# Performance work log

Hardware: AMD Instinct MI355X
Metric: run time of the kernel (lower is better)

Reference implementation:

```python
import jax, jax.numpy as jnp
import numpy as np

B, D_IN, D_H, D_OUT, E = 8192, 512, 2048, 512, 8


def setup_inputs() -> dict:
    key = jax.random.key(0)
    k = jax.random.split(key, 6)
    return {
        "x": jax.random.normal(k[0], (B, D_IN), dtype=jnp.float32),
        "groups": jax.random.randint(k[1], (B, 1), 0, E, dtype=jnp.int64),
        "W1": jax.random.normal(k[2], (E, D_IN, D_H), dtype=jnp.float32) * (1.0 / np.sqrt(D_IN)),
        "b1": jnp.zeros((E, D_H), dtype=jnp.float32),
        "W2": jax.random.normal(k[3], (E, D_H, D_OUT), dtype=jnp.float32) * (1.0 / np.sqrt(D_H)),
        "b2": jnp.zeros((E, D_OUT), dtype=jnp.float32),
    }


def reference(x, groups, W1, b1, W2, b2):
    # SubnetGate: hard one-hot routing on group column 0, then weighted
    # combine (gate value is exactly 1.0 for the selected expert).
    n_expert = W1.shape[0]
    gate = jax.nn.one_hot(groups[:, 0], n_expert, dtype=x.dtype)  # [B, E]
    out = jnp.zeros((x.shape[0], W2.shape[-1]), dtype=x.dtype)
    # Loop over the small fixed expert set (structurally distinct subnets);
    # mask-combine reproduces dispatch -> subnet -> scatter/combine exactly.
    for e in range(n_expert):
        h = jax.nn.relu(x @ W1[e] + b1[e])        # [B, D_H]
        y = h @ W2[e] + b2[e]                      # [B, D_OUT]
        out = out + gate[:, e:e + 1] * y
    return out
```

## Files before the change

kernel.cpp:

```cpp
#include <hip/hip_runtime.h>
#include <hip/hip_bf16.h>

typedef unsigned short u16;
typedef __bf16 bf16x8 __attribute__((ext_vector_type(8)));
typedef float floatx4 __attribute__((ext_vector_type(4)));
typedef unsigned short ushort8 __attribute__((ext_vector_type(8)));

#define GLOBAL_AS(p) ((const __attribute__((address_space(1))) void*)(p))
#define LDS_AS(p) ((__attribute__((address_space(3))) void*)(p))

constexpr int NB = 8192;
constexpr int DIN = 512;
constexpr int DH = 2048;
constexpr int DOUT = 512;
constexpr int NEXP = 8;
constexpr int ROWCAP = NB + NEXP * 128;
constexpr int RCAPRD = NB + NEXP * 256;
constexpr int TILE = 8192;

__device__ __forceinline__ u16 f2bf(float f) {
    unsigned u = __builtin_bit_cast(unsigned, f);
    unsigned r = u + 0x7FFFu + ((u >> 16) & 1u);
    return (u16)(r >> 16);
}

__device__ __forceinline__ int slot_off(int row, int kl) {
    return row * 64 + ((((kl >> 3) ^ (row & 7)) << 3) | (kl & 7));
}

__global__ __launch_bounds__(1024) void route_kernel(
        const int* __restrict__ groups, int* __restrict__ cnt,
        int* __restrict__ offs, int* __restrict__ perm, int* __restrict__ rpos) {
    __shared__ int wc[NEXP * 16];
    __shared__ int lcur[NEXP * 16];
    int t = threadIdx.x;
    int w = t >> 6;
    if (t < NEXP * 16) wc[t] = 0;
    __syncthreads();
    for (int i = t; i < NB; i += 1024) atomicAdd(&wc[groups[i] * 16 + w], 1);
    __syncthreads();
    if (t == 0) {
        int run = 0;
        for (int e = 0; e < NEXP; ++e) {
            offs[e] = run;
            int s = run;
            for (int j = 0; j < 16; ++j) { lcur[e * 16 + j] = s; s += wc[e * 16 + j]; }
            cnt[e] = s - run;
            run += (((s - run) + 127) >> 7) << 7;
        }
    }
    __syncthreads();
    for (int i = t; i < NB; i += 1024) {
        int e = groups[i];
        int pos = atomicAdd(&lcur[e * 16 + w], 1);
        perm[pos] = i;
        rpos[i] = pos;
    }
}

__global__ __launch_bounds__(256) void prep_kernel(
        const float* __restrict__ x, const float* __restrict__ W1,
        const float* __restrict__ W2, const int* __restrict__ rpos,
        u16* __restrict__ xsT, u16* __restrict__ w1tT, u16* __restrict__ w2tT) {
    int bx = blockIdx.x;
    int t = threadIdx.x;
    if (bx < 4096) {
        __shared__ float tile[64][65];
        bool isW1 = bx < 2048;
        int b = isW1 ? bx : bx - 2048;
        int e = b >> 8;
        int q = b & 255;
        int C = isW1 ? DH : DOUT;
        int NTP = C >> 7;
        int KTP = isW1 ? (DIN >> 6) : (DH >> 6);
        int rt = isW1 ? (q >> 5) : (q >> 3);
        int ct = isW1 ? (q & 31) : (q & 7);
        const float* s = (isW1 ? W1 : W2) + (size_t)e * (isW1 ? DIN * DH : DH * DOUT);
        u16* d = isW1 ? w1tT : w2tT;
        int r0 = rt * 64, c0 = ct * 64;
        for (int i = 0; i < 4; ++i) {
            int r = (t >> 4) + i * 16;
            int c = (t & 15) * 4;
            const float4 v = *(const float4*)&s[(size_t)(r0 + r) * C + c0 + c];
            tile[r][c] = v.x; tile[r][c + 1] = v.y; tile[r][c + 2] = v.z; tile[r][c + 3] = v.w;
        }
        __syncthreads();
        for (int i = 0; i < 2; ++i) {
            int c = (t >> 3) + i * 32;
            int r = (t & 7) * 8;
            int n = c0 + c, k = r0 + r;
            ushort8 o;
#pragma unroll
            for (int j = 0; j < 8; ++j) o[j] = f2bf(tile[r + j][c]);
            size_t off = ((size_t)(e * NTP + (n >> 7)) * KTP + (k >> 6)) * TILE
                         + slot_off(n & 127, k & 63);
            *(ushort8*)&d[off] = o;
        }
    } else {
        int r = t >> 6, lane = t & 63;
        int i = (bx - 4096) * 4 + r;
        int pos = rpos[i];
        int k = lane * 8;
        const float4 a = *(const float4*)&x[(size_t)i * DIN + k];
        const float4 b = *(const float4*)&x[(size_t)i * DIN + k + 4];
        ushort8 o;
        o[0] = f2bf(a.x); o[1] = f2bf(a.y); o[2] = f2bf(a.z); o[3] = f2bf(a.w);
        o[4] = f2bf(b.x); o[5] = f2bf(b.y); o[6] = f2bf(b.z); o[7] = f2bf(b.w);
        int lp = pos & 127;
        size_t off = (size_t)(pos >> 7) * 8 * TILE + (size_t)(k >> 6) * TILE
                     + slot_off(lp, k & 63);
        *(ushort8*)&xsT[off] = o;
    }
}


#define LDF(base, row, c0) \
    (*(const bf16x8*)&(base)[(row) * 64 + ((((c0) ^ ((row) & 7))) << 3)])

__device__ __forceinline__ void stage2(const u16* a, const u16* b,
                                       u16* buf, int soff, int doff) {
#pragma unroll
    for (int ch = 0; ch < 4; ++ch) {
        __builtin_amdgcn_global_load_lds(GLOBAL_AS(a + ch * 2048 + soff),
                                         LDS_AS(buf + ch * 2048 + doff), 16, 0, 0);
        __builtin_amdgcn_global_load_lds(GLOBAL_AS(b + ch * 2048 + soff),
                                         LDS_AS(buf + TILE + ch * 2048 + doff), 16, 0, 0);
    }
}

__device__ __forceinline__ void compute_step(const u16* At, const u16* Bt,
                                             int arow, int brow,
                                             floatx4 (&acc)[4][4], int q, int li) {
#pragma unroll
    for (int s = 0; s < 2; ++s) {
        int c0 = s * 4 + q;
        bf16x8 bfr[4];
#pragma unroll
        for (int fn = 0; fn < 4; ++fn) bfr[fn] = LDF(Bt, brow + fn * 16 + li, c0);
#pragma unroll
        for (int fm = 0; fm < 4; ++fm) {
            bf16x8 af = LDF(At, arow + fm * 16 + li, c0);
#pragma unroll
            for (int fn = 0; fn < 4; ++fn)
                acc[fm][fn] = __builtin_amdgcn_mfma_f32_16x16x32_bf16(
                    af, bfr[fn], acc[fm][fn], 0, 0, 0);
        }
    }
}

template <int KT>
__device__ __forceinline__ void gemm_core2(const u16* a0, const u16* b0,
                                           u16* sm, floatx4 (&acc)[4][4],
                                           int arow, int brow,
                                           int q, int li, int soff, int doff) {
    stage2(a0, b0, sm, soff, doff);
    int cur = 0;
#pragma unroll 1
    for (int kt = 0; kt < KT; ++kt) {
        asm volatile("s_waitcnt vmcnt(0)" ::: "memory");
        __builtin_amdgcn_s_barrier();
        __builtin_amdgcn_sched_barrier(0);
        if (kt + 1 < KT)
            stage2(a0 + (size_t)(kt + 1) * TILE, b0 + (size_t)(kt + 1) * TILE,
                   sm + (size_t)(cur ^ 1) * 2 * TILE, soff, doff);
        const u16* At = sm + (size_t)(cur * 2 + 0) * TILE;
        const u16* Bt = sm + (size_t)(cur * 2 + 1) * TILE;
        compute_step(At, Bt, arow, brow, acc, q, li);
        __builtin_amdgcn_sched_barrier(0);
        __builtin_amdgcn_s_barrier();
        cur ^= 1;
    }
}

__global__ __launch_bounds__(256) __attribute__((amdgpu_waves_per_eu(2)))
void gemm_a(const u16* __restrict__ At, const u16* __restrict__ Bt,
            const float* __restrict__ bias, u16* __restrict__ hsT,
            const int* __restrict__ cnt, const int* __restrict__ offs) {
    __shared__ u16 sm[2 * 2 * TILE];
    int bx = blockIdx.x;
    int e = bx & 7;
    int r = bx >> 3;
    int nt = r & 15;
    int mt0 = r >> 4;
    int count = cnt[e];
    int base128 = offs[e] >> 7;
    int tid = threadIdx.x;
    int w = tid >> 6, l = tid & 63, q = l >> 4, li = l & 15;
    int wm = w >> 1, wn = w & 1;
    int arow = wm * 64, brow = wn * 64;
    int soff = tid * 8, doff = w * 512;
#pragma unroll 1
    for (int mt = mt0; mt * 128 < count; mt += 9) {
        const u16* a0 = At + (size_t)((base128 + mt) * 8) * TILE;
        const u16* b0 = Bt + (size_t)((e * 16 + nt) * 8) * TILE;
        floatx4 acc[4][4];
#pragma unroll
        for (int a = 0; a < 4; ++a)
#pragma unroll
            for (int b = 0; b < 4; ++b) acc[a][b] = (floatx4)0.0f;

        gemm_core2<8>(a0, b0, sm, acc, arow, brow, q, li, soff, doff);

        float bv[4];
#pragma unroll
        for (int fn = 0; fn < 4; ++fn)
            bv[fn] = bias[(size_t)e * DH + nt * 128 + wn * 64 + fn * 16 + li];
        u16* img = sm + (size_t)w * 4096;
#pragma unroll
        for (int fm = 0; fm < 4; ++fm)
#pragma unroll
            for (int fn = 0; fn < 4; ++fn)
#pragma unroll
                for (int rr = 0; rr < 4; ++rr) {
                    float v = acc[fm][fn][rr] + bv[fn];
                    v = v > 0.0f ? v : 0.0f;
                    int row = fm * 16 + q * 4 + rr;
                    int col = fn * 16 + li;
                    img[row * 64 + ((((col >> 3) ^ (row & 7)) << 3) | (col & 7))] = f2bf(v);
                }
        u16* dst = hsT + ((size_t)(base128 + mt) * 32 + nt * 2 + wn) * TILE + wm * 4096;
#pragma unroll
        for (int j = 0; j < 8; ++j)
            *(ushort8*)&dst[j * 512 + l * 8] = *(const ushort8*)&img[j * 512 + l * 8];
        __syncthreads();
    }
}

__global__ __launch_bounds__(256) __attribute__((amdgpu_waves_per_eu(2)))
void gemm_b(const u16* __restrict__ At, const u16* __restrict__ Bt,
            float* __restrict__ ps, const int* __restrict__ cnt,
            const int* __restrict__ offs) {
    __shared__ u16 sm[2 * 2 * TILE];
    int bx = blockIdx.x;
    int e = bx & 7;
    int r = bx >> 3;
    int nt = r & 3;
    int ks = (r >> 2) & 1;
    int mt0 = r >> 3;
    int count = cnt[e];
    int seg = offs[e];
    int base128 = seg >> 7;
    int tid = threadIdx.x;
    int w = tid >> 6, l = tid & 63, q = l >> 4, li = l & 15;
    int wm = w >> 1, wn = w & 1;
    int arow = wm * 64, brow = wn * 64;
    int soff = tid * 8, doff = w * 512;
#pragma unroll 1
    for (int mt = mt0; mt * 128 < count; mt += 9) {
        const u16* a0 = At + (size_t)((base128 + mt) * 32 + ks * 16) * TILE;
        const u16* b0 = Bt + (size_t)((e * 4 + nt) * 32 + ks * 16) * TILE;
        floatx4 acc[4][4];
#pragma unroll
        for (int a = 0; a < 4; ++a)
#pragma unroll
            for (int b = 0; b < 4; ++b) acc[a][b] = (floatx4)0.0f;

        gemm_core2<16>(a0, b0, sm, acc, arow, brow, q, li, soff, doff);

        float* pbase = ps + ((size_t)ks * ROWCAP + seg + (size_t)mt * 128) * DOUT;
#pragma unroll
        for (int fn = 0; fn < 4; ++fn) {
            int col = nt * 128 + wn * 64 + fn * 16 + li;
#pragma unroll
            for (int fm = 0; fm < 4; ++fm) {
                int row0 = wm * 64 + fm * 16 + q * 4;
#pragma unroll
                for (int rr = 0; rr < 4; ++rr)
                    pbase[(size_t)(row0 + rr) * DOUT + col] = acc[fm][fn][rr];
            }
        }
        __syncthreads();
    }
}

__global__ __launch_bounds__(256) void reduce_b(
        const float* __restrict__ ps, const int* __restrict__ rpos,
        const int* __restrict__ groups, const float* __restrict__ b2,
        float* __restrict__ out) {
    int idx = blockIdx.x * 256 + threadIdx.x;
    int i = idx >> 7;
    int c = (idx & 127) * 4;
    int pos = rpos[i];
    int g = groups[i];
    const float4 v0 = *(const float4*)&ps[(size_t)pos * DOUT + c];
    const float4 v1 = *(const float4*)&ps[((size_t)ROWCAP + pos) * DOUT + c];
    const float4 bb = *(const float4*)&b2[(size_t)g * DOUT + c];
    float4 o;
    o.x = v0.x + v1.x + bb.x; o.y = v0.y + v1.y + bb.y;
    o.z = v0.z + v1.z + bb.z; o.w = v0.w + v1.w + bb.w;
    *(float4*)&out[(size_t)i * DOUT + c] = o;
}

extern "C" void kernel_launch(void* const* d_in, const int* in_sizes, int n_in,
                              void* d_out, int out_size, void* d_ws, size_t ws_size,
                              hipStream_t stream) {
    const float* x = (const float*)d_in[0];
    const int* groups = (const int*)d_in[1];
    const float* W1 = (const float*)d_in[2];
    const float* b1 = (const float*)d_in[3];
    const float* W2 = (const float*)d_in[4];
    const float* b2 = (const float*)d_in[5];
    float* out = (float*)d_out;

    char* ws = (char*)d_ws;
    size_t o = 0;
    auto alloc = [&](size_t bytes) {
        void* p = ws + o;
        o = (o + bytes + 255) & ~(size_t)255;
        return p;
    };
    int* cnt = (int*)alloc(NEXP * 4);
    int* offs = (int*)alloc(NEXP * 4);
    int* perm = (int*)alloc((size_t)ROWCAP * 4);
    int* rpos = (int*)alloc((size_t)NB * 4);
    u16* xsT = (u16*)alloc((size_t)(RCAPRD / 128) * 8 * TILE * 2);
    u16* w1tT = (u16*)alloc((size_t)NEXP * DIN * DH * 2);
    u16* w2tT = (u16*)alloc((size_t)NEXP * DH * DOUT * 2);
    u16* hsT = (u16*)alloc((size_t)(RCAPRD / 128) * 32 * TILE * 2);
    float* ps = (float*)alloc((size_t)2 * ROWCAP * DOUT * 4);

    route_kernel<<<1, 1024, 0, stream>>>(groups, cnt, offs, perm, rpos);
    prep_kernel<<<6144, 256, 0, stream>>>(x, W1, W2, rpos, xsT, w1tT, w2tT);
    gemm_a<<<NEXP * 16 * 9, 256, 0, stream>>>(xsT, w1tT, b1, hsT, cnt, offs);
    gemm_b<<<NEXP * 4 * 2 * 9, 256, 0, stream>>>(hsT, w2tT, ps, cnt, offs);
    reduce_b<<<(NB * (DOUT / 4)) / 256, 256, 0, stream>>>(ps, rpos, groups, b2, out);
}
```

Baseline: 206.0 us.

## Drop split-K in second GEMM and fuse bias plus scatter into its epilogue

```diff
diff --git a/kernel.cpp b/kernel.cpp
--- a/kernel.cpp
+++ b/kernel.cpp
@@ -113,9 +113,28 @@
     }
 }
 
-
 #define LDF(base, row, c0) \
     (*(const bf16x8*)&(base)[(row) * 64 + ((((c0) ^ ((row) & 7))) << 3)])
+
+__device__ __forceinline__ void compute_step(const u16* At, const u16* Bt,
+                                             int arow, int brow,
+                                             floatx4 (&acc)[4][4], int q, int li) {
+#pragma unroll
+    for (int s = 0; s < 2; ++s) {
+        int c0 = s * 4 + q;
+        bf16x8 bfr[4];
+#pragma unroll
+        for (int fn = 0; fn < 4; ++fn) bfr[fn] = LDF(Bt, brow + fn * 16 + li, c0);
+#pragma unroll
+        for (int fm = 0; fm < 4; ++fm) {
+            bf16x8 af = LDF(At, arow + fm * 16 + li, c0);
+#pragma unroll
+            for (int fn = 0; fn < 4; ++fn)
+                acc[fm][fn] = __builtin_amdgcn_mfma_f32_16x16x32_bf16(
+                    af, bfr[fn], acc[fm][fn], 0, 0, 0);
+        }
+    }
+}
 
 __device__ __forceinline__ void stage2(const u16* a, const u16* b,
                                        u16* buf, int soff, int doff) {
@@ -125,26 +144,6 @@
                                          LDS_AS(buf + ch * 2048 + doff), 16, 0, 0);
         __builtin_amdgcn_global_load_lds(GLOBAL_AS(b + ch * 2048 + soff),
                                          LDS_AS(buf + TILE + ch * 2048 + doff), 16, 0, 0);
-    }
-}
-
-__device__ __forceinline__ void compute_step(const u16* At, const u16* Bt,
-                                             int arow, int brow,
-                                             floatx4 (&acc)[4][4], int q, int li) {
-#pragma unroll
-    for (int s = 0; s < 2; ++s) {
-        int c0 = s * 4 + q;
-        bf16x8 bfr[4];
-#pragma unroll
-        for (int fn = 0; fn < 4; ++fn) bfr[fn] = LDF(Bt, brow + fn * 16 + li, c0);
-#pragma unroll
-        for (int fm = 0; fm < 4; ++fm) {
-            bf16x8 af = LDF(At, arow + fm * 16 + li, c0);
-#pragma unroll
-            for (int fn = 0; fn < 4; ++fn)
-                acc[fm][fn] = __builtin_amdgcn_mfma_f32_16x16x32_bf16(
-                    af, bfr[fn], acc[fm][fn], 0, 0, 0);
-        }
     }
 }
 
@@ -226,69 +225,84 @@
     }
 }
 
-__global__ __launch_bounds__(256) __attribute__((amdgpu_waves_per_eu(2)))
+__device__ __forceinline__ void stage_f(const u16* a, const u16* b,
+                                        u16* buf, int soff, int doff) {
+#pragma unroll
+    for (int ch = 0; ch < 4; ++ch)
+        __builtin_amdgcn_global_load_lds(GLOBAL_AS(a + ch * 1024 + soff),
+                                         LDS_AS(buf + ch * 1024 + doff), 16, 0, 0);
+#pragma unroll
+    for (int ch = 0; ch < 8; ++ch)
+        __builtin_amdgcn_global_load_lds(GLOBAL_AS(b + ch * 1024 + soff),
+                                         LDS_AS(buf + 4096 + ch * 1024 + doff), 16, 0, 0);
+}
+
+__global__ __launch_bounds__(128) __attribute__((amdgpu_waves_per_eu(2)))
 void gemm_b(const u16* __restrict__ At, const u16* __restrict__ Bt,
-            float* __restrict__ ps, const int* __restrict__ cnt,
+            const float* __restrict__ b2, const int* __restrict__ perm,
+            float* __restrict__ out, const int* __restrict__ cnt,
             const int* __restrict__ offs) {
-    __shared__ u16 sm[2 * 2 * TILE];
+    __shared__ u16 sm[2 * 12288];
     int bx = blockIdx.x;
     int e = bx & 7;
     int r = bx >> 3;
     int nt = r & 3;
-    int ks = (r >> 2) & 1;
-    int mt0 = r >> 3;
+    int mt0 = r >> 2;
     int count = cnt[e];
     int seg = offs[e];
     int base128 = seg >> 7;
     int tid = threadIdx.x;
     int w = tid >> 6, l = tid & 63, q = l >> 4, li = l & 15;
-    int wm = w >> 1, wn = w & 1;
-    int arow = wm * 64, brow = wn * 64;
     int soff = tid * 8, doff = w * 512;
+    int brow = w * 64;
 #pragma unroll 1
-    for (int mt = mt0; mt * 128 < count; mt += 9) {
-        const u16* a0 = At + (size_t)((base128 + mt) * 32 + ks * 16) * TILE;
-        const u16* b0 = Bt + (size_t)((e * 4 + nt) * 32 + ks * 16) * TILE;
+    for (int mt = mt0; mt * 64 < count; mt += 18) {
+        const u16* a0 = At + (size_t)((base128 + (mt >> 1)) * 32) * TILE + (mt & 1) * 4096;
+        const u16* b0 = Bt + (size_t)((e * 4 + nt) * 32) * TILE;
         floatx4 acc[4][4];
 #pragma unroll
         for (int a = 0; a < 4; ++a)
 #pragma unroll
             for (int b = 0; b < 4; ++b) acc[a][b] = (floatx4)0.0f;
 
-        gemm_core2<16>(a0, b0, sm, acc, arow, brow, q, li, soff, doff);
-
-        float* pbase = ps + ((size_t)ks * ROWCAP + seg + (size_t)mt * 128) * DOUT;
-#pragma unroll
-        for (int fn = 0; fn < 4; ++fn) {
-            int col = nt * 128 + wn * 64 + fn * 16 + li;
-#pragma unroll
-            for (int fm = 0; fm < 4; ++fm) {
-                int row0 = wm * 64 + fm * 16 + q * 4;
-#pragma unroll
-                for (int rr = 0; rr < 4; ++rr)
-                    pbase[(size_t)(row0 + rr) * DOUT + col] = acc[fm][fn][rr];
+        stage_f(a0, b0, sm, soff, doff);
+        int cur = 0;
+#pragma unroll 1
+        for (int kt = 0; kt < 32; ++kt) {
+            asm volatile("s_waitcnt vmcnt(0)" ::: "memory");
+            __builtin_amdgcn_s_barrier();
+            __builtin_amdgcn_sched_barrier(0);
+            if (kt + 1 < 32)
+                stage_f(a0 + (size_t)(kt + 1) * TILE, b0 + (size_t)(kt + 1) * TILE,
+                        sm + (size_t)(cur ^ 1) * 12288, soff, doff);
+            const u16* Atile = sm + (size_t)cur * 12288;
+            const u16* Btile = Atile + 4096;
+            compute_step(Atile, Btile, 0, brow, acc, q, li);
+            __builtin_amdgcn_sched_barrier(0);
+            __builtin_amdgcn_s_barrier();
+            cur ^= 1;
+        }
+
+        float bv[4];
+#pragma unroll
+        for (int fn = 0; fn < 4; ++fn)
+            bv[fn] = b2[(size_t)e * DOUT + nt * 128 + brow + fn * 16 + li];
+        int rowbase = mt * 64;
+#pragma unroll
+        for (int fm = 0; fm < 4; ++fm)
+#pragma unroll
+            for (int rr = 0; rr < 4; ++rr) {
+                int lr = fm * 16 + q * 4 + rr;
+                if (rowbase + lr < count) {
+                    int gi = perm[seg + rowbase + lr];
+                    float* orow = out + (size_t)gi * DOUT + nt * 128 + brow;
+#pragma unroll
+                    for (int fn = 0; fn < 4; ++fn)
+                        orow[fn * 16 + li] = acc[fm][fn][rr] + bv[fn];
+                }
             }
-        }
         __syncthreads();
     }
-}
-
-__global__ __launch_bounds__(256) void reduce_b(
-        const float* __restrict__ ps, const int* __restrict__ rpos,
-        const int* __restrict__ groups, const float* __restrict__ b2,
-        float* __restrict__ out) {
-    int idx = blockIdx.x * 256 + threadIdx.x;
-    int i = idx >> 7;
-    int c = (idx & 127) * 4;
-    int pos = rpos[i];
-    int g = groups[i];
-    const float4 v0 = *(const float4*)&ps[(size_t)pos * DOUT + c];
-    const float4 v1 = *(const float4*)&ps[((size_t)ROWCAP + pos) * DOUT + c];
-    const float4 bb = *(const float4*)&b2[(size_t)g * DOUT + c];
-    float4 o;
-    o.x = v0.x + v1.x + bb.x; o.y = v0.y + v1.y + bb.y;
-    o.z = v0.z + v1.z + bb.z; o.w = v0.w + v1.w + bb.w;
-    *(float4*)&out[(size_t)i * DOUT + c] = o;
 }
 
 extern "C" void kernel_launch(void* const* d_in, const int* in_sizes, int n_in,
@@ -317,11 +331,9 @@
     u16* w1tT = (u16*)alloc((size_t)NEXP * DIN * DH * 2);
     u16* w2tT = (u16*)alloc((size_t)NEXP * DH * DOUT * 2);
     u16* hsT = (u16*)alloc((size_t)(RCAPRD / 128) * 32 * TILE * 2);
-    float* ps = (float*)alloc((size_t)2 * ROWCAP * DOUT * 4);
 
     route_kernel<<<1, 1024, 0, stream>>>(groups, cnt, offs, perm, rpos);
     prep_kernel<<<6144, 256, 0, stream>>>(x, W1, W2, rpos, xsT, w1tT, w2tT);
     gemm_a<<<NEXP * 16 * 9, 256, 0, stream>>>(xsT, w1tT, b1, hsT, cnt, offs);
-    gemm_b<<<NEXP * 4 * 2 * 9, 256, 0, stream>>>(hsT, w2tT, ps, cnt, offs);
-    reduce_b<<<(NB * (DOUT / 4)) / 256, 256, 0, stream>>>(ps, rpos, groups, b2, out);
-}
+    gemm_b<<<NEXP * 4 * 18, 128, 0, stream>>>(hsT, w2tT, b2, perm, out, cnt, offs);
+}
```

Measured after the change: 197.5 us. 1.04x faster.
